# Kernel tuning notes

Hardware: AMD Instinct MI355X
Metric: run time of the kernel (lower is better)

## Reference

```python
import jax, jax.numpy as jnp
import numpy as np

EPS = 1e-5

def _conv3x3(x, w, b):
    # NCHW, OIHW, 3x3 stride 1 pad 1
    y = jax.lax.conv_general_dilated(x, w, window_strides=(1, 1),
                                     padding=((1, 1), (1, 1)),
                                     dimension_numbers=('NCHW', 'OIHW', 'NCHW'))
    return y + b[None, :, None, None]

def _pool_upsample(x, k):
    # adaptive avg pool to (H/k, W/k) then nearest block-upsample back
    B, C, H, W = x.shape
    p = x.reshape(B, C, H // k, k, W // k, k).mean(axis=(3, 5))
    return jnp.repeat(jnp.repeat(p, k, axis=2), k, axis=3)

def setup_inputs() -> dict:
    key = jax.random.key(0)
    ks = jax.random.split(key, 12)
    B, C, H, W = 32, 8, 300, 300
    d = {
        'x': jax.random.normal(ks[0], (B, C, H, W), jnp.float32),
        'w5': jax.random.normal(ks[1], (8, 16, 3, 3), jnp.float32) * 0.1,
        'b5': jnp.zeros((8,), jnp.float32),
        'w10': jax.random.normal(ks[2], (8, 16, 3, 3), jnp.float32) * 0.1,
        'b10': jnp.zeros((8,), jnp.float32),
        'w15': jax.random.normal(ks[3], (8, 16, 3, 3), jnp.float32) * 0.1,
        'b15': jnp.zeros((8,), jnp.float32),
        'gw': jax.random.normal(ks[4], (8, 24, 3, 3), jnp.float32) * 0.1,
        'gb': jnp.zeros((8,), jnp.float32),
        'mw': jax.random.normal(ks[5], (8, 24, 3, 3), jnp.float32) * 0.1,
        'mb': jnp.zeros((8,), jnp.float32),
        'gamma': jnp.ones((8,), jnp.float32),
        'beta': jnp.zeros((8,), jnp.float32),
    }
    return d

def reference(x, w5, b5, w10, b10, w15, b15, gw, gb, mw, mb, gamma, beta):
    up5 = _pool_upsample(x, 5)    # [B,8,300,300]
    up10 = _pool_upsample(x, 10)
    up15 = _pool_upsample(x, 15)
    c5 = _conv3x3(jnp.concatenate([x, up5], axis=1), w5, b5)
    c10 = _conv3x3(jnp.concatenate([x, up10], axis=1), w10, b10)
    c15 = _conv3x3(jnp.concatenate([x, up15], axis=1), w15, b15)
    g_in = jnp.concatenate([c5, c10, c15], axis=1)  # [B,24,H,W]
    # gated conv, activation=None: conv(g_in) * sigmoid(mask_conv(g_in))
    y = _conv3x3(g_in, gw, gb) * jax.nn.sigmoid(_conv3x3(g_in, mw, mb))
    # batch norm (training-mode batch stats, biased var, as torch default)
    mean = y.mean(axis=(0, 2, 3), keepdims=True)
    var = ((y - mean) ** 2).mean(axis=(0, 2, 3), keepdims=True)
    y = (y - mean) * jax.lax.rsqrt(var + EPS)
    return y * gamma[None, :, None, None] + beta[None, :, None, None]
```

## Files before the change

kernel.cpp:

```cpp
#include <hip/hip_runtime.h>
#include <math.h>

typedef __bf16 bfrag __attribute__((ext_vector_type(8)));
typedef float f32x4 __attribute__((ext_vector_type(4)));

#define BN 32
#define HH 300
#define WW 300
#define HW 90000
#define NPX (BN * HW)

#define GX 10
#define GY 19

#define P5I_BYTE_OFF   0
#define P10I_BYTE_OFF  1843200
#define P15I_BYTE_OFF  2304000
#define CWB_BYTE_OFF   2508800
#define GWB_BYTE_OFF   2524160
#define STAT_BYTE_OFF  2531328
#define SS_BYTE_OFF    2539520

__device__ __forceinline__ short f2bf(float f) {
    union { float f; unsigned u; } v;
    v.f = f;
    unsigned r = v.u + 0x7FFF + ((v.u >> 16) & 1);
    return (short)(r >> 16);
}

__global__ void k_setup(const float* __restrict__ w5, const float* __restrict__ w10,
                        const float* __restrict__ w15, const float* __restrict__ gw,
                        const float* __restrict__ mw, short* __restrict__ cBg,
                        short* __restrict__ gBg, double* __restrict__ stats) {
    int t = threadIdx.x;
    for (int idx = t; idx < 7680; idx += 256) {
        int s = idx / 2560, rem = idx % 2560;
        int n = rem / 160, r2 = rem % 160;
        int tap = r2 / 16, ci = r2 % 16;
        float v = 0.f;
        if (n < 8 && tap < 9) {
            const float* W = (s == 0) ? w5 : ((s == 1) ? w10 : w15);
            v = W[(n * 16 + ci) * 9 + tap];
        }
        cBg[idx] = f2bf(v);
    }
    for (int idx = t; idx < 3584; idx += 256) {
        int n = idx / 224, r2 = idx % 224;
        int blk = r2 / 8, cj = r2 % 8;
        float v = 0.f;
        if (blk < 27) {
            int tap = blk / 3, ci24 = (blk % 3) * 8 + cj;
            if (n < 8) v = gw[(n * 24 + ci24) * 9 + tap];
            else       v = mw[((n - 8) * 24 + ci24) * 9 + tap];
        }
        gBg[idx] = f2bf(v);
    }
    for (int idx = t; idx < 16 * 64; idx += 256) stats[idx] = 0.0;
}

__global__ void k_pool(const float* __restrict__ x, unsigned short* __restrict__ p5i,
                       unsigned short* __restrict__ p10i, unsigned short* __restrict__ p15i) {
    int bc = blockIdx.x;
    int b = bc >> 3, c = bc & 7;
    const float* xp = x + (size_t)bc * HW;
    __shared__ float p5[3600];

    for (int cell = threadIdx.x; cell < 3600; cell += 256) {
        int pi = cell / 60, pj = cell % 60;
        const float* rp = xp + pi * 5 * WW + pj * 5;
        float s = 0.f;
#pragma unroll
        for (int u = 0; u < 5; u++)
#pragma unroll
            for (int v = 0; v < 5; v++) s += rp[u * WW + v];
        float m = s * 0.04f;
        p5[cell] = m;
        p5i[((size_t)b * 3600 + cell) * 8 + c] = (unsigned short)f2bf(m);
    }
    __syncthreads();
    for (int cell = threadIdx.x; cell < 900; cell += 256) {
        int pi = cell / 30, pj = cell % 30;
        float s = p5[(2 * pi) * 60 + 2 * pj] + p5[(2 * pi) * 60 + 2 * pj + 1] +
                  p5[(2 * pi + 1) * 60 + 2 * pj] + p5[(2 * pi + 1) * 60 + 2 * pj + 1];
        p10i[((size_t)b * 900 + cell) * 8 + c] = (unsigned short)f2bf(s * 0.25f);
    }
    for (int cell = threadIdx.x; cell < 400; cell += 256) {
        int pi = cell / 20, pj = cell % 20;
        float s = 0.f;
#pragma unroll
        for (int u = 0; u < 3; u++)
#pragma unroll
            for (int v = 0; v < 3; v++) s += p5[(3 * pi + u) * 60 + 3 * pj + v];
        p15i[((size_t)b * 400 + cell) * 8 + c] = (unsigned short)f2bf(s * (1.f / 9.f));
    }
}

template <int K, int PW>
__device__ __forceinline__ void up_load(const unsigned short* __restrict__ pooled,
                                        int b, int r0, int c0, int t, uint4* v) {
#pragma unroll
    for (int it = 0; it < 3; it++) {
        int idx = t + 256 * it;
        uint4 val = {0u, 0u, 0u, 0u};
        if (idx < 720) {
            int i = idx / 36, j = idx - i * 36;
            int ra = r0 - 2 + i, ca = c0 - 2 + j;
            if (ra >= 0 && ra < HH && ca >= 0 && ca < WW) {
                int pi = (int)((unsigned)ra / K);
                int pj = (int)((unsigned)ca / K);
                val = *(const uint4*)&pooled[((size_t)b * (PW * PW) + pi * PW + pj) * 8];
            }
        }
        v[it] = val;
    }
}

__device__ __forceinline__ void up_store(short* xu, int t, const uint4* v) {
#pragma unroll
    for (int it = 0; it < 3; it++) {
        int idx = t + 256 * it;
        if (idx < 720) *(uint4*)&xu[idx * 16 + 8] = v[it];
    }
}

__device__ __forceinline__ void c_phase(const short* xu, short* cwS,
                                        const unsigned short* __restrict__ cBs,
                                        const float* __restrict__ bias, int s,
                                        int r0, int c0, int lane, int wid) {
    const int n = lane & 15, quad = lane >> 4;
    const int qh = quad >> 1, ql = quad & 1;
    bfrag bfr[5];
    int tapoff[5];
#pragma unroll
    for (int km = 0; km < 5; km++) {
        int tapw = km * 2 + qh;
        int tapa = (tapw > 8) ? 8 : tapw;
        bfr[km] = *(const bfrag*)&cBs[(n * 10 + tapw) * 16 + ql * 8];
        tapoff[km] = ((tapa / 3) * 36 + tapa % 3) * 16;
    }
    float bo = (n < 8) ? bias[n] : 0.f;
    for (int g = wid; g < 39; g += 4) {
        int px = g * 16 + n;
        if (px > 611) px = 611;
        int rp = px / 34, cp = px - rp * 34;
        int off0 = (rp * 36 + cp) * 16 + ql * 8;
        f32x4 acc = {0.f, 0.f, 0.f, 0.f};
#pragma unroll
        for (int km = 0; km < 5; km++)
            acc = __builtin_amdgcn_mfma_f32_16x16x32_bf16(
                *(const bfrag*)&xu[off0 + tapoff[km]], bfr[km], acc, 0, 0, 0);
        if (n < 8) {
#pragma unroll
            for (int reg = 0; reg < 4; reg++) {
                int px2 = g * 16 + quad * 4 + reg;
                if (px2 < 612) {
                    int r2 = px2 / 34, c2 = px2 - r2 * 34;
                    int ra = r0 - 1 + r2, ca = c0 - 1 + c2;
                    float v = acc[reg] + bo;
                    if (ra < 0 || ra >= HH || ca < 0 || ca >= WW) v = 0.f;
                    cwS[(r2 * 34 + c2) * 24 + s * 8 + n] = f2bf(v);
                }
            }
        }
    }
}

__global__ __launch_bounds__(256, 3) void k_fused(
    const float* __restrict__ x,
    const unsigned short* __restrict__ p5i, const unsigned short* __restrict__ p10i,
    const unsigned short* __restrict__ p15i,
    const unsigned short* __restrict__ cBg, const unsigned short* __restrict__ gBg,
    const float* __restrict__ b5, const float* __restrict__ b10, const float* __restrict__ b15,
    const float* __restrict__ gb, const float* __restrict__ mb,
    float* __restrict__ out, double* __restrict__ stats) {
    __shared__ __align__(16) short xu[20 * 36 * 16];
    __shared__ __align__(16) short cwS[18 * 34 * 24];

    const int b = blockIdx.z;
    const int r0 = blockIdx.y * 16, c0 = blockIdx.x * 32;
    const int t = threadIdx.x, lane = t & 63, wid = t >> 6;

    uint4 upv[3];
    up_load<5, 60>(p5i, b, r0, c0, t, upv);

    for (int idx = t; idx < 2880; idx += 256) {
        int cp = idx / 720, rem = idx % 720;
        int i = rem / 36, j = rem % 36;
        int ra = r0 - 2 + i, ca = c0 - 2 + j;
        float v0 = 0.f, v1 = 0.f;
        if (ra >= 0 && ra < HH && ca >= 0 && ca < WW) {
            size_t base = ((size_t)(b * 8 + 2 * cp) * HH + ra) * WW + ca;
            v0 = x[base];
            v1 = x[base + HW];
        }
        unsigned p = (unsigned short)f2bf(v0) | ((unsigned)(unsigned short)f2bf(v1) << 16);
        *(unsigned*)&xu[(i * 36 + j) * 16 + 2 * cp] = p;
    }
    up_store(xu, t, upv);
    __syncthreads();

    c_phase(xu, cwS, cBg, b5, 0, r0, c0, lane, wid);
    up_load<10, 30>(p10i, b, r0, c0, t, upv);
    __syncthreads();
    up_store(xu, t, upv);
    __syncthreads();

    c_phase(xu, cwS, cBg + 2560, b10, 1, r0, c0, lane, wid);
    up_load<15, 20>(p15i, b, r0, c0, t, upv);
    __syncthreads();
    up_store(xu, t, upv);
    __syncthreads();

    c_phase(xu, cwS, cBg + 5120, b15, 2, r0, c0, lane, wid);
    __syncthreads();

    const int n = lane & 15, quad = lane >> 4;
    bfrag gfr[7];
    int goff[7];
#pragma unroll
    for (int km = 0; km < 7; km++) {
        int blkw = km * 4 + quad;
        int blka = (blkw > 26) ? 26 : blkw;
        gfr[km] = *(const bfrag*)&gBg[(n * 28 + blkw) * 8];
        int tap = blka / 3, cig = blka - tap * 3;
        goff[km] = ((tap / 3) * 34 + tap % 3) * 24 + cig * 8;
    }
    float gbv = (n < 8) ? gb[n] : 0.f;
    float mbv = (n < 8) ? mb[n] : 0.f;
    float ls = 0.f, ls2 = 0.f;

    for (int g = wid; g < 32; g += 4) {
        int px = g * 16 + n;
        int rr = px >> 5, cc2 = px & 31;
        int off0 = (rr * 34 + cc2) * 24;
        f32x4 acc = {0.f, 0.f, 0.f, 0.f};
#pragma unroll
        for (int km = 0; km < 7; km++)
            acc = __builtin_amdgcn_mfma_f32_16x16x32_bf16(
                *(const bfrag*)&cwS[off0 + goff[km]], gfr[km], acc, 0, 0, 0);
#pragma unroll
        for (int reg = 0; reg < 4; reg++) {
            float other = __shfl_xor(acc[reg], 8);
            if (n < 8) {
                int px2 = g * 16 + quad * 4 + reg;
                int rr2 = px2 >> 5, cc3 = px2 & 31;
                int ra = r0 + rr2, ca = c0 + cc3;
                if (ra < HH && ca < WW) {
                    float G = acc[reg] + gbv, M = other + mbv;
                    float y = G / (1.f + __expf(-M));
                    out[((size_t)(b * 8 + n) * HH + ra) * WW + ca] = y;
                    ls += y;
                    ls2 += y * y;
                }
            }
        }
    }
    ls += __shfl_xor(ls, 16);
    ls += __shfl_xor(ls, 32);
    ls2 += __shfl_xor(ls2, 16);
    ls2 += __shfl_xor(ls2, 32);
    if (lane < 8) {
        int hash = (blockIdx.x + GX * blockIdx.y + GX * GY * blockIdx.z) & 63;
        atomicAdd(&stats[lane * 64 + hash], (double)ls);
        atomicAdd(&stats[(8 + lane) * 64 + hash], (double)ls2);
    }
}

__global__ void k_stats(const double* __restrict__ stats, const float* __restrict__ gamma,
                        const float* __restrict__ beta, float* __restrict__ ss) {
    __shared__ double tot[16];
    int t = threadIdx.x;
    if (t < 16) {
        double s = 0.0;
        for (int i = 0; i < 64; i++) s += stats[t * 64 + i];
        tot[t] = s;
    }
    __syncthreads();
    if (t < 8) {
        double N = (double)NPX;
        double mean = tot[t] / N;
        double var = tot[8 + t] / N - mean * mean;
        double scale = (double)gamma[t] / sqrt(var + 1e-5);
        ss[t] = (float)scale;
        ss[8 + t] = (float)((double)beta[t] - mean * scale);
    }
}

__global__ void k_norm(float* __restrict__ out, const float* __restrict__ ss) {
    int i = blockIdx.x * 256 + threadIdx.x;
    if (i < (BN * 8 * HW) / 4) {
        int plane = (i * 4) / HW;
        int ch = plane & 7;
        float sc = ss[ch], sh = ss[8 + ch];
        float4* p = (float4*)out + i;
        float4 v = *p;
        v.x = v.x * sc + sh;
        v.y = v.y * sc + sh;
        v.z = v.z * sc + sh;
        v.w = v.w * sc + sh;
        *p = v;
    }
}

extern "C" void kernel_launch(void* const* d_in, const int* in_sizes, int n_in,
                              void* d_out, int out_size, void* d_ws, size_t ws_size,
                              hipStream_t stream) {
    const float* x = (const float*)d_in[0];
    const float* w5 = (const float*)d_in[1];
    const float* b5 = (const float*)d_in[2];
    const float* w10 = (const float*)d_in[3];
    const float* b10 = (const float*)d_in[4];
    const float* w15 = (const float*)d_in[5];
    const float* b15 = (const float*)d_in[6];
    const float* gw = (const float*)d_in[7];
    const float* gb = (const float*)d_in[8];
    const float* mw = (const float*)d_in[9];
    const float* mb = (const float*)d_in[10];
    const float* gamma = (const float*)d_in[11];
    const float* beta = (const float*)d_in[12];

    float* out = (float*)d_out;
    unsigned short* p5i = (unsigned short*)((char*)d_ws + P5I_BYTE_OFF);
    unsigned short* p10i = (unsigned short*)((char*)d_ws + P10I_BYTE_OFF);
    unsigned short* p15i = (unsigned short*)((char*)d_ws + P15I_BYTE_OFF);
    short* cBg = (short*)((char*)d_ws + CWB_BYTE_OFF);
    short* gBg = (short*)((char*)d_ws + GWB_BYTE_OFF);
    double* stats = (double*)((char*)d_ws + STAT_BYTE_OFF);
    float* ss = (float*)((char*)d_ws + SS_BYTE_OFF);

    k_setup<<<1, 256, 0, stream>>>(w5, w10, w15, gw, mw, cBg, gBg, stats);
    k_pool<<<BN * 8, 256, 0, stream>>>(x, p5i, p10i, p15i);
    dim3 grid(GX, GY, BN);
    k_fused<<<grid, 256, 0, stream>>>(x, p5i, p10i, p15i,
                                      (const unsigned short*)cBg, (const unsigned short*)gBg,
                                      b5, b10, b15, gb, mb, out, stats);
    k_stats<<<1, 64, 0, stream>>>(stats, gamma, beta, ss);
    k_norm<<<(BN * 8 * HW / 4 + 255) / 256, 256, 0, stream>>>(out, ss);
}
```

Baseline: 426.9 us.

## Split pooling into parallel pool5 and downsample kernels, vectorize x tile loads

Replaces the per-(batch,channel) pooling kernel, which had only 256 blocks, with a per-cell 5x5 pooling kernel and a second kernel that derives the 10x10 and 15x15 pools from the bf16 5x5 result. This raises parallelism for the pooling stage at the cost of an extra launch and slightly different rounding. Also loads x pairs as float2 in the fused kernel and removes per-element divisions in the conv epilogue.

```diff
diff --git a/kernel.cpp b/kernel.cpp
--- a/kernel.cpp
+++ b/kernel.cpp
@@ -26,6 +26,12 @@
     v.f = f;
     unsigned r = v.u + 0x7FFF + ((v.u >> 16) & 1);
     return (short)(r >> 16);
+}
+
+__device__ __forceinline__ float bf2f(unsigned short s) {
+    union { unsigned u; float f; } v;
+    v.u = ((unsigned)s) << 16;
+    return v.f;
 }
 
 __global__ void k_setup(const float* __restrict__ w5, const float* __restrict__ w10,
@@ -58,39 +64,46 @@
     for (int idx = t; idx < 16 * 64; idx += 256) stats[idx] = 0.0;
 }
 
-__global__ void k_pool(const float* __restrict__ x, unsigned short* __restrict__ p5i,
-                       unsigned short* __restrict__ p10i, unsigned short* __restrict__ p15i) {
-    int bc = blockIdx.x;
+__global__ void k_pool5(const float* __restrict__ x, unsigned short* __restrict__ p5i) {
+    int id = blockIdx.x * 256 + threadIdx.x;
+    int bc = id / 3600, cell = id % 3600;
     int b = bc >> 3, c = bc & 7;
-    const float* xp = x + (size_t)bc * HW;
-    __shared__ float p5[3600];
-
-    for (int cell = threadIdx.x; cell < 3600; cell += 256) {
-        int pi = cell / 60, pj = cell % 60;
-        const float* rp = xp + pi * 5 * WW + pj * 5;
+    int pi = cell / 60, pj = cell % 60;
+    const float* rp = x + (size_t)bc * HW + pi * 5 * WW + pj * 5;
+    float s = 0.f;
+#pragma unroll
+    for (int u = 0; u < 5; u++)
+#pragma unroll
+        for (int v = 0; v < 5; v++) s += rp[u * WW + v];
+    p5i[((size_t)b * 3600 + cell) * 8 + c] = (unsigned short)f2bf(s * 0.04f);
+}
+
+__global__ void k_poolD(const unsigned short* __restrict__ p5i,
+                        unsigned short* __restrict__ p10i,
+                        unsigned short* __restrict__ p15i) {
+    int id = blockIdx.x * 256 + threadIdx.x;
+    if (id < 230400) {
+        int bc = id / 900, cell = id % 900;
+        int b = bc >> 3, c = bc & 7;
+        int pi = cell / 30, pj = cell % 30;
+        const unsigned short* base = p5i + ((size_t)b * 3600) * 8 + c;
+        float s = bf2f(base[((2 * pi) * 60 + 2 * pj) * 8]) +
+                  bf2f(base[((2 * pi) * 60 + 2 * pj + 1) * 8]) +
+                  bf2f(base[((2 * pi + 1) * 60 + 2 * pj) * 8]) +
+                  bf2f(base[((2 * pi + 1) * 60 + 2 * pj + 1) * 8]);
+        p10i[((size_t)b * 900 + cell) * 8 + c] = (unsigned short)f2bf(s * 0.25f);
+    } else if (id < 332800) {
+        int id2 = id - 230400;
+        int bc = id2 / 400, cell = id2 % 400;
+        int b = bc >> 3, c = bc & 7;
+        int pi = cell / 20, pj = cell % 20;
+        const unsigned short* base = p5i + ((size_t)b * 3600) * 8 + c;
         float s = 0.f;
 #pragma unroll
-        for (int u = 0; u < 5; u++)
-#pragma unroll
-            for (int v = 0; v < 5; v++) s += rp[u * WW + v];
-        float m = s * 0.04f;
-        p5[cell] = m;
-        p5i[((size_t)b * 3600 + cell) * 8 + c] = (unsigned short)f2bf(m);
-    }
-    __syncthreads();
-    for (int cell = threadIdx.x; cell < 900; cell += 256) {
-        int pi = cell / 30, pj = cell % 30;
-        float s = p5[(2 * pi) * 60 + 2 * pj] + p5[(2 * pi) * 60 + 2 * pj + 1] +
-                  p5[(2 * pi + 1) * 60 + 2 * pj] + p5[(2 * pi + 1) * 60 + 2 * pj + 1];
-        p10i[((size_t)b * 900 + cell) * 8 + c] = (unsigned short)f2bf(s * 0.25f);
-    }
-    for (int cell = threadIdx.x; cell < 400; cell += 256) {
-        int pi = cell / 20, pj = cell % 20;
-        float s = 0.f;
-#pragma unroll
         for (int u = 0; u < 3; u++)
 #pragma unroll
-            for (int v = 0; v < 3; v++) s += p5[(3 * pi + u) * 60 + 3 * pj + v];
+            for (int v = 0; v < 3; v++)
+                s += bf2f(base[((3 * pi + u) * 60 + 3 * pj + v) * 8]);
         p15i[((size_t)b * 400 + cell) * 8 + c] = (unsigned short)f2bf(s * (1.f / 9.f));
     }
 }
@@ -150,16 +163,18 @@
             acc = __builtin_amdgcn_mfma_f32_16x16x32_bf16(
                 *(const bfrag*)&xu[off0 + tapoff[km]], bfr[km], acc, 0, 0, 0);
         if (n < 8) {
+            int px2 = g * 16 + quad * 4;
+            int r2 = px2 / 34, c2 = px2 - r2 * 34;
 #pragma unroll
             for (int reg = 0; reg < 4; reg++) {
-                int px2 = g * 16 + quad * 4 + reg;
-                if (px2 < 612) {
-                    int r2 = px2 / 34, c2 = px2 - r2 * 34;
+                if (px2 + reg < 612) {
                     int ra = r0 - 1 + r2, ca = c0 - 1 + c2;
                     float v = acc[reg] + bo;
                     if (ra < 0 || ra >= HH || ca < 0 || ca >= WW) v = 0.f;
                     cwS[(r2 * 34 + c2) * 24 + s * 8 + n] = f2bf(v);
                 }
+                c2++;
+                if (c2 == 34) { c2 = 0; r2++; }
             }
         }
     }
@@ -183,18 +198,22 @@
     uint4 upv[3];
     up_load<5, 60>(p5i, b, r0, c0, t, upv);
 
-    for (int idx = t; idx < 2880; idx += 256) {
-        int cp = idx / 720, rem = idx % 720;
-        int i = rem / 36, j = rem % 36;
+    for (int idx = t; idx < 1440; idx += 256) {
+        int cp = idx / 360, rem = idx % 360;
+        int i = rem / 18, jp = rem % 18;
+        int j = 2 * jp;
         int ra = r0 - 2 + i, ca = c0 - 2 + j;
-        float v0 = 0.f, v1 = 0.f;
-        if (ra >= 0 && ra < HH && ca >= 0 && ca < WW) {
+        float2 v0 = {0.f, 0.f}, v1 = {0.f, 0.f};
+        if (ra >= 0 && ra < HH && ca >= 0 && ca <= WW - 2) {
             size_t base = ((size_t)(b * 8 + 2 * cp) * HH + ra) * WW + ca;
-            v0 = x[base];
-            v1 = x[base + HW];
-        }
-        unsigned p = (unsigned short)f2bf(v0) | ((unsigned)(unsigned short)f2bf(v1) << 16);
-        *(unsigned*)&xu[(i * 36 + j) * 16 + 2 * cp] = p;
+            v0 = *(const float2*)&x[base];
+            v1 = *(const float2*)&x[base + HW];
+        }
+        unsigned pA = (unsigned short)f2bf(v0.x) | ((unsigned)(unsigned short)f2bf(v1.x) << 16);
+        unsigned pB = (unsigned short)f2bf(v0.y) | ((unsigned)(unsigned short)f2bf(v1.y) << 16);
+        int px = i * 36 + j;
+        *(unsigned*)&xu[px * 16 + 2 * cp] = pA;
+        *(unsigned*)&xu[(px + 1) * 16 + 2 * cp] = pB;
     }
     up_store(xu, t, upv);
     __syncthreads();
@@ -329,7 +348,8 @@
     float* ss = (float*)((char*)d_ws + SS_BYTE_OFF);
 
     k_setup<<<1, 256, 0, stream>>>(w5, w10, w15, gw, mw, cBg, gBg, stats);
-    k_pool<<<BN * 8, 256, 0, stream>>>(x, p5i, p10i, p15i);
+    k_pool5<<<3600, 256, 0, stream>>>(x, p5i);
+    k_poolD<<<1300, 256, 0, stream>>>(p5i, p10i, p15i);
     dim3 grid(GX, GY, BN);
     k_fused<<<grid, 256, 0, stream>>>(x, p5i, p10i, p15i,
                                       (const unsigned short*)cBg, (const unsigned short*)gBg,
```

After: 417.8 us. 2.1% less time.
